# Kernel tuning notes

Hardware: AMD Instinct MI355X
Metric: run time of the kernel (lower is better)

## Reference

```python
import jax, jax.numpy as jnp
import numpy as np

B, N, E = 2, 2048, 1024   # batch, seq_len, embed_dim (= hidden_dim)
H, HD = 16, 64            # num_heads, head_dim


def setup_inputs() -> dict:
    key = jax.random.key(0)
    ks = jax.random.split(key, 6)
    w = lambda k: jax.random.normal(k, (E, E), jnp.float32) * 0.02
    return {
        "x": jax.random.normal(ks[0], (B, N, E), jnp.float32),
        "Wq": w(ks[1]), "bq": jnp.zeros((E,), jnp.float32),
        "Wk": w(ks[2]), "bk": jnp.zeros((E,), jnp.float32),
        "Wv": w(ks[3]), "bv": jnp.zeros((E,), jnp.float32),
        "Wu": w(ks[4]), "bu": jnp.zeros((E,), jnp.float32),
        "Wo": w(ks[5]), "bo": jnp.zeros((E,), jnp.float32),
        "ln_g": jnp.ones((E,), jnp.float32),
        "ln_b": jnp.zeros((E,), jnp.float32),
    }


def reference(x, Wq, bq, Wk, bk, Wv, bv, Wu, bu, Wo, bo, ln_g, ln_b):
    # projections (torch Linear: x @ W.T + b)
    q = x @ Wq.T + bq
    k = x @ Wk.T + bk
    v = jax.nn.silu(x @ Wv.T + bv)   # uv_act = swish
    u = jax.nn.silu(x @ Wu.T + bu)
    # split heads: [B, N, H*HD] -> [B, H, N, HD]
    split = lambda t: t.reshape(B, N, H, HD).transpose(0, 2, 1, 3)
    q, k, v = split(q), split(k), split(v)
    # non-softmax attention: ReLU on scaled energy (no causal mask)
    energy = jnp.einsum("bhnd,bhmd->bhnm", q, k) / jnp.float32(np.sqrt(HD))
    energy = jax.nn.relu(energy)
    out = jnp.einsum("bhnm,bhmd->bhnd", energy, v)
    # merge heads: [B, H, N, HD] -> [B, N, H*HD]
    out = out.transpose(0, 2, 1, 3).reshape(B, N, H * HD)
    # layernorm over hidden_dim
    mu = out.mean(-1, keepdims=True)
    var = out.var(-1, keepdims=True)
    out = (out - mu) * jax.lax.rsqrt(var + 1e-5) * ln_g + ln_b
    # gate and output projection
    out = u * out
    return out @ Wo.T + bo
```

## Files before the change

### kernel.cpp

```cpp
#include <hip/hip_runtime.h>
#include <stdint.h>

typedef unsigned short u16;
typedef __attribute__((ext_vector_type(8))) short short8;
typedef __attribute__((ext_vector_type(4))) short short4v;
typedef __attribute__((ext_vector_type(4))) float floatx4;
typedef __attribute__((ext_vector_type(4))) int intx4;

#define B_ 2
#define N_ 2048
#define E_ 1024
#define H_ 16
#define HD_ 64
#define M_TOT (B_ * N_)

__device__ __forceinline__ float bf2f(u16 h) {
    union { unsigned u; float f; } c; c.u = ((unsigned)h) << 16; return c.f;
}
__device__ __forceinline__ u16 f2bf(float f) {
    union { float f; unsigned u; } c; c.f = f;
    unsigned r = c.u + 0x7FFFu + ((c.u >> 16) & 1u);
    return (u16)(r >> 16);
}
__device__ __forceinline__ float silu_f(float x) { return x / (1.f + __expf(-x)); }

template <typename T> __device__ __forceinline__ void store_out(T* p, float v);
template <> __device__ __forceinline__ void store_out<u16>(u16* p, float v)    { *p = f2bf(v); }
template <> __device__ __forceinline__ void store_out<float>(float* p, float v) { *p = v; }

__device__ __forceinline__ void gll16(const void* g, void* l) {
    __builtin_amdgcn_global_load_lds(
        (const __attribute__((address_space(1))) void*)g,
        (__attribute__((address_space(3))) void*)l,
        16, 0, 0);
}

__device__ __forceinline__ short4v relu_pack(floatx4 s) {
    union { float f; unsigned u; } c0, c1, c2, c3;
    c0.f = fmaxf(s[0], 0.f); c1.f = fmaxf(s[1], 0.f);
    c2.f = fmaxf(s[2], 0.f); c3.f = fmaxf(s[3], 0.f);
    unsigned lo = __builtin_amdgcn_perm(c1.u + 0x8000u, c0.u + 0x8000u, 0x07060302);
    unsigned hi = __builtin_amdgcn_perm(c3.u + 0x8000u, c2.u + 0x8000u, 0x07060302);
    union { unsigned v[2]; short4v s4; } r; r.v[0] = lo; r.v[1] = hi;
    return r.s4;
}

__launch_bounds__(256, 4)
__global__ void cvt6(const float* __restrict__ s0, const float* __restrict__ s1,
                     const float* __restrict__ s2, const float* __restrict__ s3,
                     const float* __restrict__ s4, const float* __restrict__ s5,
                     u16* __restrict__ d0, u16* __restrict__ d1,
                     u16* __restrict__ d2, u16* __restrict__ d3,
                     u16* __restrict__ d4, u16* __restrict__ d5)
{
    const int z = blockIdx.z;
    if (z > 0 && blockIdx.x >= E_ * E_ / 2048) return;
    const float* src = (z == 0) ? s0 : (z == 1) ? s1 : (z == 2) ? s2
                     : (z == 3) ? s3 : (z == 4) ? s4 : s5;
    u16* dst         = (z == 0) ? d0 : (z == 1) ? d1 : (z == 2) ? d2
                     : (z == 3) ? d3 : (z == 4) ? d4 : d5;
    const int i = (blockIdx.x * 256 + threadIdx.x) * 8;
    floatx4 a = *(const floatx4*)(src + i);
    floatx4 b = *(const floatx4*)(src + i + 4);
    union { u16 h[8]; intx4 v; } o;
    o.h[0] = f2bf(a[0]); o.h[1] = f2bf(a[1]); o.h[2] = f2bf(a[2]); o.h[3] = f2bf(a[3]);
    o.h[4] = f2bf(b[0]); o.h[5] = f2bf(b[1]); o.h[6] = f2bf(b[2]); o.h[7] = f2bf(b[3]);
    *(intx4*)(dst + i) = o.v;
}

template <typename OutT>
__launch_bounds__(256, 2)
__global__ void gemm4(const u16* __restrict__ A,
                      const u16* __restrict__ W0, const u16* __restrict__ W1,
                      const u16* __restrict__ W2, const u16* __restrict__ W3,
                      const float* __restrict__ bi0, const float* __restrict__ bi1,
                      const float* __restrict__ bi2, const float* __restrict__ bi3,
                      OutT* __restrict__ O0, OutT* __restrict__ O1,
                      OutT* __restrict__ O2, OutT* __restrict__ O3,
                      int actmask, int scalemask, int K)
{
    __shared__ u16 a_lds[128 * 32];
    __shared__ u16 b_lds[128 * 32];

    const int lin = blockIdx.x + blockIdx.y * 8 + blockIdx.z * 256;
    const int swz = (lin & 7) * 128 + (lin >> 3);
    const int z   = swz >> 8;
    const int by  = (swz >> 3) & 31;
    const int bx  = swz & 7;

    const u16* W    = (z == 0) ? W0 : (z == 1) ? W1 : (z == 2) ? W2 : W3;
    const float* Bi = (z == 0) ? bi0 : (z == 1) ? bi1 : (z == 2) ? bi2 : bi3;
    OutT* Out       = (z == 0) ? O0 : (z == 1) ? O1 : (z == 2) ? O2 : O3;
    const bool act = (actmask >> z) & 1;
    const float osc = ((scalemask >> z) & 1) ? 0.125f : 1.0f;

    const int t    = threadIdx.x;
    const int wave = t >> 6, lane = t & 63, quad = lane >> 4, l16 = lane & 15;
    const int wm = wave >> 1, wn = wave & 1;
    const int m0 = by * 128;
    const int n0 = bx * 128;

    floatx4 acc[4][4];
    const floatx4 fz = {0.f, 0.f, 0.f, 0.f};
    for (int i = 0; i < 4; i++)
        for (int j = 0; j < 4; j++) acc[i][j] = fz;

    const int ar = t >> 2;
    const int ac = (t & 3) * 8;
    const u16* Ag0 = A + (size_t)(m0 + ar) * K + ac;
    const u16* Ag1 = A + (size_t)(m0 + 64 + ar) * K + ac;
    const u16* Bg0 = W + (size_t)(n0 + ar) * K + ac;
    const u16* Bg1 = W + (size_t)(n0 + 64 + ar) * K + ac;
    u16* al0 = a_lds + wave * 512;
    u16* al1 = a_lds + 2048 + wave * 512;
    u16* bl0 = b_lds + wave * 512;
    u16* bl1 = b_lds + 2048 + wave * 512;

    for (int k0 = 0; k0 < K; k0 += 32) {
        __syncthreads();
        gll16(Ag0 + k0, al0);
        gll16(Ag1 + k0, al1);
        gll16(Bg0 + k0, bl0);
        gll16(Bg1 + k0, bl1);
        __syncthreads();

        short8 af[4], bfr[4];
        for (int i = 0; i < 4; i++)
            af[i]  = *(const short8*)&a_lds[(wm * 64 + i * 16 + l16) * 32 + quad * 8];
        for (int j = 0; j < 4; j++)
            bfr[j] = *(const short8*)&b_lds[(wn * 64 + j * 16 + l16) * 32 + quad * 8];
        for (int i = 0; i < 4; i++)
            for (int j = 0; j < 4; j++)
                acc[i][j] = __builtin_amdgcn_mfma_f32_16x16x32_bf16(af[i], bfr[j], acc[i][j], 0, 0, 0);
    }

    float bias_v[4];
    for (int j = 0; j < 4; j++) bias_v[j] = Bi[n0 + wn * 64 + j * 16 + l16];

    for (int i = 0; i < 4; i++) {
        const int row = m0 + wm * 64 + i * 16 + quad * 4;
        for (int j = 0; j < 4; j++) {
            const int col = n0 + wn * 64 + j * 16 + l16;
            for (int r = 0; r < 4; r++) {
                float v = acc[i][j][r] + bias_v[j];
                if (act) v = silu_f(v);
                v *= osc;
                store_out<OutT>(&Out[(size_t)(row + r) * E_ + col], v);
            }
        }
    }
}

__launch_bounds__(256, 2)
__global__ void gemm_out(const u16* __restrict__ A, const u16* __restrict__ W,
                         const float* __restrict__ Bi, float* __restrict__ Out,
                         int K)
{
    __shared__ u16 a_lds[3][64 * 32];
    __shared__ u16 b_lds[3][128 * 32];

    const int t    = threadIdx.x;
    const int wave = t >> 6, lane = t & 63, quad = lane >> 4, l16 = lane & 15;
    const int m0 = blockIdx.y * 64;
    const int n0 = blockIdx.x * 128;

    floatx4 acc[4][2];
    const floatx4 fz = {0.f, 0.f, 0.f, 0.f};
    for (int i = 0; i < 4; i++)
        for (int j = 0; j < 2; j++) acc[i][j] = fz;

    const int ar = t >> 2;
    const int ac = (t & 3) * 8;
    const u16* Ag0 = A + (size_t)(m0 + ar) * K + ac;
    const u16* Bg0 = W + (size_t)(n0 + ar) * K + ac;
    const u16* Bg1 = W + (size_t)(n0 + 64 + ar) * K + ac;

    const int nt = K / 32;

#define GO_STAGE(tt, bi) {                                      \
        gll16(Ag0 + (tt) * 32, &a_lds[bi][wave * 512]);         \
        gll16(Bg0 + (tt) * 32, &b_lds[bi][wave * 512]);         \
        gll16(Bg1 + (tt) * 32, &b_lds[bi][2048 + wave * 512]); }

    GO_STAGE(0, 0);
    GO_STAGE(1, 1);
    asm volatile("s_waitcnt vmcnt(3)" ::: "memory");
    __builtin_amdgcn_s_barrier();

    for (int tt = 0; tt < nt; tt++) {
        const int bi = tt % 3;
        if (tt + 2 < nt) {
            GO_STAGE(tt + 2, (tt + 2) % 3);
        }
        short8 af[4], bfr[2];
#pragma unroll
        for (int i = 0; i < 4; i++)
            af[i]  = *(const short8*)&a_lds[bi][(i * 16 + l16) * 32 + quad * 8];
#pragma unroll
        for (int j = 0; j < 2; j++)
            bfr[j] = *(const short8*)&b_lds[bi][(wave * 32 + j * 16 + l16) * 32 + quad * 8];
#pragma unroll
        for (int i = 0; i < 4; i++)
#pragma unroll
            for (int j = 0; j < 2; j++)
                acc[i][j] = __builtin_amdgcn_mfma_f32_16x16x32_bf16(af[i], bfr[j], acc[i][j], 0, 0, 0);
        if (tt + 2 < nt) {
            asm volatile("s_waitcnt vmcnt(3)" ::: "memory");
        } else {
            asm volatile("s_waitcnt vmcnt(0)" ::: "memory");
        }
        __builtin_amdgcn_s_barrier();
    }
#undef GO_STAGE

    float bias_v[2];
    for (int j = 0; j < 2; j++) bias_v[j] = Bi[n0 + wave * 32 + j * 16 + l16];

    for (int i = 0; i < 4; i++) {
        const int row = m0 + i * 16 + quad * 4;
        for (int j = 0; j < 2; j++) {
            const int col = n0 + wave * 32 + j * 16 + l16;
            for (int r = 0; r < 4; r++)
                Out[(size_t)(row + r) * E_ + col] = acc[i][j][r] + bias_v[j];
        }
    }
}

#define LK 72
#define LV 72
#define KSPLIT 2
#define KCHUNK (N_ / KSPLIT)
#define NKT (KCHUNK / 64)

__launch_bounds__(256, 2)
__global__ void attn(const u16* __restrict__ Q, const u16* __restrict__ Kk,
                     const u16* __restrict__ V,
                     u16* __restrict__ P0, u16* __restrict__ P1)
{
    __shared__ u16 k_lds[2][64 * LK];
    __shared__ u16 v_lds[2][64 * LV];

    const int lin = blockIdx.x + blockIdx.y * 8 + blockIdx.z * 256;
    const int swz = (lin & 7) * 64 + (lin >> 3);
    const int z   = swz >> 8;
    const int bh  = (swz >> 3) & 31;
    const int qb  = swz & 7;

    const int b = bh >> 4, h = bh & 15;
    u16* __restrict__ Oa = (z == 0) ? P0 : P1;
    const int key_base = z * KCHUNK;

    const int t = threadIdx.x;
    const int wave = t >> 6, lane = t & 63, quad = lane >> 4, l16 = lane & 15;
    const int q0 = qb * 256 + wave * 64;
    const size_t base = (size_t)b * N_ * E_ + h * HD_;

    short8 aq[4][2];
    for (int mi = 0; mi < 4; mi++)
        for (int ks = 0; ks < 2; ks++)
            aq[mi][ks] = *(const short8*)(Q + base + (size_t)(q0 + mi * 16 + l16) * E_ + ks * 32 + quad * 8);

    floatx4 o[4][4];
    const floatx4 fz = {0.f, 0.f, 0.f, 0.f};
    for (int mi = 0; mi < 4; mi++)
        for (int nd = 0; nd < 4; nd++) o[mi][nd] = fz;

    const int srow = t >> 2, sseg = (t & 3) * 16;
    const int prow = (srow & 32) + (((srow >> 2) & 1) << 4)
                   + (((srow >> 3) & 3) << 2) + (srow & 3);
    const u16* Ksrc = Kk + base + (size_t)(key_base + srow) * E_ + sseg;
    const u16* Vsrc = V + base + (size_t)(key_base + srow) * E_ + sseg;
    const int kofs = prow * LK + sseg;

    intx4 kv0 = *(const intx4*)(Ksrc);
    intx4 kv1 = *(const intx4*)(Ksrc + 8);
    intx4 vv0 = *(const intx4*)(Vsrc);
    intx4 vv1 = *(const intx4*)(Vsrc + 8);
    {
        *(intx4*)(&k_lds[0][kofs])     = kv0;
        *(intx4*)(&k_lds[0][kofs + 8]) = kv1;
        const u16* v0p = (const u16*)&vv0;
        const u16* v1p = (const u16*)&vv1;
        for (int i = 0; i < 8; i++) {
            v_lds[0][(sseg + i) * LV + srow]     = v0p[i];
            v_lds[0][(sseg + 8 + i) * LV + srow] = v1p[i];
        }
    }

    for (int kt = 0; kt < NKT; kt++) {
        __syncthreads();
        const int cur = kt & 1;

        if (kt + 1 < NKT) {
            const u16* kg = Ksrc + (size_t)((kt + 1) * 64) * E_;
            const u16* vg = Vsrc + (size_t)((kt + 1) * 64) * E_;
            kv0 = *(const intx4*)(kg);
            kv1 = *(const intx4*)(kg + 8);
            vv0 = *(const intx4*)(vg);
            vv1 = *(const intx4*)(vg + 8);
        }

        for (int g = 0; g < 2; g++) {
            short8 ka[2][2];
            for (int tp = 0; tp < 2; tp++)
                for (int ks = 0; ks < 2; ks++)
                    ka[tp][ks] = *(const short8*)&k_lds[cur][(g * 32 + tp * 16 + l16) * LK + ks * 32 + quad * 8];
            short8 bv[4];
            for (int nd = 0; nd < 4; nd++)
                bv[nd] = *(const short8*)&v_lds[cur][(nd * 16 + l16) * LV + g * 32 + quad * 8];

            for (int mi = 0; mi < 4; mi++) {
                floatx4 c0 = __builtin_amdgcn_mfma_f32_16x16x32_bf16(ka[0][0], aq[mi][0], fz, 0, 0, 0);
                c0 = __builtin_amdgcn_mfma_f32_16x16x32_bf16(ka[0][1], aq[mi][1], c0, 0, 0, 0);
                floatx4 c1 = __builtin_amdgcn_mfma_f32_16x16x32_bf16(ka[1][0], aq[mi][0], fz, 0, 0, 0);
                c1 = __builtin_amdgcn_mfma_f32_16x16x32_bf16(ka[1][1], aq[mi][1], c1, 0, 0, 0);
                union { short4v h[2]; short8 s8; } sf;
                sf.h[0] = relu_pack(c0);
                sf.h[1] = relu_pack(c1);
                for (int nd = 0; nd < 4; nd++)
                    o[mi][nd] = __builtin_amdgcn_mfma_f32_16x16x32_bf16(sf.s8, bv[nd], o[mi][nd], 0, 0, 0);
            }
        }

        if (kt + 1 < NKT) {
            const int nxt = cur ^ 1;
            *(intx4*)(&k_lds[nxt][kofs])     = kv0;
            *(intx4*)(&k_lds[nxt][kofs + 8]) = kv1;
            const u16* v0p = (const u16*)&vv0;
            const u16* v1p = (const u16*)&vv1;
            for (int i = 0; i < 8; i++) {
                v_lds[nxt][(sseg + i) * LV + srow]     = v0p[i];
                v_lds[nxt][(sseg + 8 + i) * LV + srow] = v1p[i];
            }
        }
    }

    for (int mi = 0; mi < 4; mi++)
        for (int nd = 0; nd < 4; nd++)
            for (int r = 0; r < 4; r++)
                Oa[(size_t)(b * N_ + q0 + mi * 16 + quad * 4 + r) * E_ + h * HD_ + nd * 16 + l16] =
                    f2bf(o[mi][nd][r]);
}

__launch_bounds__(256, 4)
__global__ void ln_gate(const u16* __restrict__ P0, const u16* __restrict__ P1,
                        const u16* __restrict__ U,
                        const float* __restrict__ G, const float* __restrict__ Bb,
                        u16* __restrict__ Out)
{
    const int row = blockIdx.x;
    const int t = threadIdx.x;
    const size_t idx = (size_t)row * E_ + t * 4;
    const short4v a0 = *(const short4v*)(P0 + idx);
    const short4v a1 = *(const short4v*)(P1 + idx);
    floatx4 v;
    for (int i = 0; i < 4; i++)
        v[i] = bf2f((u16)a0[i]) + bf2f((u16)a1[i]);
    float s  = v[0] + v[1] + v[2] + v[3];
    float ss = v[0] * v[0] + v[1] * v[1] + v[2] * v[2] + v[3] * v[3];
    for (int off = 32; off; off >>= 1) {
        s  += __shfl_down(s, off, 64);
        ss += __shfl_down(ss, off, 64);
    }
    __shared__ float red[8];
    const int wave = t >> 6, lane = t & 63;
    if (lane == 0) { red[wave] = s; red[4 + wave] = ss; }
    __syncthreads();
    const float S  = red[0] + red[1] + red[2] + red[3];
    const float SS = red[4] + red[5] + red[6] + red[7];
    const float mu  = S * (1.f / E_);
    const float var = SS * (1.f / E_) - mu * mu;
    const float rstd = rsqrtf(var + 1e-5f);

    short4v outv;
    for (int i = 0; i < 4; i++) {
        const int e = t * 4 + i;
        float y = (v[i] - mu) * rstd * G[e] + Bb[e];
        y *= bf2f(U[idx + i]);
        outv[i] = (short)f2bf(y);
    }
    *(short4v*)(Out + idx) = outv;
}

extern "C" void kernel_launch(void* const* d_in, const int* in_sizes, int n_in,
                              void* d_out, int out_size, void* d_ws, size_t ws_size,
                              hipStream_t stream)
{
    const float* x   = (const float*)d_in[0];
    const float* Wq  = (const float*)d_in[1];
    const float* bq  = (const float*)d_in[2];
    const float* Wk  = (const float*)d_in[3];
    const float* bk  = (const float*)d_in[4];
    const float* Wv  = (const float*)d_in[5];
    const float* bv  = (const float*)d_in[6];
    const float* Wu  = (const float*)d_in[7];
    const float* bu  = (const float*)d_in[8];
    const float* Wo  = (const float*)d_in[9];
    const float* bo  = (const float*)d_in[10];
    const float* lng = (const float*)d_in[11];
    const float* lnb = (const float*)d_in[12];

    char* ws = (char*)d_ws;
    u16*  qw  = (u16*)(ws);
    u16*  kw  = (u16*)(ws + 8388608);
    u16*  vw  = (u16*)(ws + 16777216);
    u16*  uw  = (u16*)(ws + 25165824);
    u16*  p0  = (u16*)(ws + 33554432);
    u16*  p1  = (u16*)(ws + 41943040);
    u16*  xb  = (u16*)(ws + 50331648);
    u16*  wbq = (u16*)(ws + 58720256);
    u16*  wbk = (u16*)(ws + 60817408);
    u16*  wbv = (u16*)(ws + 62914560);
    u16*  wbu = (u16*)(ws + 65011712);
    u16*  wbo = (u16*)(ws + 67108864);
    u16*  gw  = (u16*)(ws);

    float* out = (float*)d_out;

    cvt6<<<dim3(M_TOT * E_ / 2048, 1, 6), dim3(256, 1, 1), 0, stream>>>(
        x, Wq, Wk, Wv, Wu, Wo, xb, wbq, wbk, wbv, wbu, wbo);
    gemm4<u16><<<dim3(8, 32, 4), dim3(256, 1, 1), 0, stream>>>(
        xb, wbq, wbk, wbv, wbu, bq, bk, bv, bu, qw, kw, vw, uw, 0xC, 0x1, E_);
    attn<<<dim3(N_ / 256, B_ * H_, KSPLIT), dim3(256, 1, 1), 0, stream>>>(qw, kw, vw, p0, p1);
    ln_gate<<<dim3(M_TOT, 1, 1), dim3(256, 1, 1), 0, stream>>>(p0, p1, uw, lng, lnb, gw);
    gemm_out<<<dim3(E_ / 128, M_TOT / 64, 1), dim3(256, 1, 1), 0, stream>>>(gw, wbo, bo, out, E_);
}
```

Measured before the change: 213.4 us.

## Split QKVU projection into large-tile Q/K GEMM and raise attention key split

```diff
diff --git a/kernel.cpp b/kernel.cpp
--- a/kernel.cpp
+++ b/kernel.cpp
@@ -68,6 +68,127 @@
     *(intx4*)(dst + i) = o.v;
 }
 
+#define NT8 (E_ / 64)
+
+__launch_bounds__(512, 2)
+__global__ void gemm8p2(const u16* __restrict__ A,
+                        const u16* __restrict__ W0, const u16* __restrict__ W1,
+                        const float* __restrict__ bi0, const float* __restrict__ bi1,
+                        u16* __restrict__ O0, u16* __restrict__ O1,
+                        int scalemask)
+{
+    __shared__ u16 lds[65536];
+
+    const int z = blockIdx.z;
+    const u16* Wp   = z ? W1 : W0;
+    const float* Bi = z ? bi1 : bi0;
+    u16* Out        = z ? O1 : O0;
+    const float osc = ((scalemask >> z) & 1) ? 0.125f : 1.0f;
+
+    const int tid = threadIdx.x;
+    const int wid = tid >> 6, lane = tid & 63, quad = lane >> 4, l16 = lane & 15;
+    const int wm = wid >> 2, wn = wid & 3;
+    const int m0 = blockIdx.y * 256;
+    const int n0 = blockIdx.x * 256;
+
+    const int swz = ((l16 >> 3) & 1) * 16;
+    const int raA = wm * 8192 + l16 * 32 + ((quad * 8) ^ swz);
+    const int raB = (wn >> 1) * 8192 + ((wn & 1) * 64 + l16) * 32 + ((quad * 8) ^ swz);
+
+    const int srow_s = tid >> 2;
+    const int sce = ((tid & 3) * 8) ^ (((tid >> 5) & 1) * 16);
+    const u16* As = A  + (size_t)(m0 + srow_s) * E_ + sce;
+    const u16* Bs = Wp + (size_t)(n0 + srow_s) * E_ + sce;
+
+#define ST_A8(t, h, bufx) if ((t) < NT8) {                                                      \
+        gll16(As + (size_t)(h)*128*E_ + (t)*64,      &lds[(bufx)*16384 + (h)*8192 + wid*512]);  \
+        gll16(As + (size_t)(h)*128*E_ + (t)*64 + 32, &lds[(bufx)*16384 + (h)*8192 + 4096 + wid*512]); }
+#define ST_B8(t, h, bufx) if ((t) < NT8) {                                                      \
+        gll16(Bs + (size_t)(h)*128*E_ + (t)*64,      &lds[32768 + (bufx)*16384 + (h)*8192 + wid*512]);  \
+        gll16(Bs + (size_t)(h)*128*E_ + (t)*64 + 32, &lds[32768 + (bufx)*16384 + (h)*8192 + 4096 + wid*512]); }
+
+    floatx4 acc[8][4];
+    const floatx4 fz = {0.f, 0.f, 0.f, 0.f};
+#pragma unroll
+    for (int mi = 0; mi < 8; mi++)
+#pragma unroll
+        for (int bn = 0; bn < 4; bn++) acc[mi][bn] = fz;
+
+    short8 af[8][2], bfr[2][2];
+
+#define RD_A8(mlo, bufx)                                                               \
+    _Pragma("unroll")                                                                  \
+    for (int mi = 0; mi < 4; mi++) {                                                   \
+        af[(mlo)+mi][0] = *(const short8*)&lds[(bufx)*16384 + raA + ((mlo)+mi)*512];   \
+        af[(mlo)+mi][1] = *(const short8*)&lds[(bufx)*16384 + raA + 4096 + ((mlo)+mi)*512]; }
+#define RD_B8(blo, bufx)                                                               \
+    _Pragma("unroll")                                                                  \
+    for (int bn = 0; bn < 2; bn++) {                                                   \
+        bfr[bn][0] = *(const short8*)&lds[32768 + (bufx)*16384 + raB + ((blo)+bn)*512];   \
+        bfr[bn][1] = *(const short8*)&lds[32768 + (bufx)*16384 + raB + 4096 + ((blo)+bn)*512]; }
+#define MF8(mlo, blo)                                                                  \
+    _Pragma("unroll")                                                                  \
+    for (int mi = 0; mi < 4; mi++)                                                     \
+        _Pragma("unroll")                                                              \
+        for (int bn = 0; bn < 2; bn++) {                                               \
+            acc[(mlo)+mi][(blo)+bn] = __builtin_amdgcn_mfma_f32_16x16x32_bf16(         \
+                af[(mlo)+mi][0], bfr[bn][0], acc[(mlo)+mi][(blo)+bn], 0, 0, 0);        \
+            acc[(mlo)+mi][(blo)+bn] = __builtin_amdgcn_mfma_f32_16x16x32_bf16(         \
+                af[(mlo)+mi][1], bfr[bn][1], acc[(mlo)+mi][(blo)+bn], 0, 0, 0); }
+
+    ST_A8(0, 0, 0); ST_A8(0, 1, 0); ST_B8(0, 0, 0); ST_B8(0, 1, 0);
+    ST_A8(1, 0, 1);
+    asm volatile("s_waitcnt vmcnt(2)" ::: "memory");
+    __builtin_amdgcn_s_barrier();
+
+    for (int t = 0; t < NT8; t++) {
+        const int buf = t & 1, ob = buf ^ 1;
+        RD_A8(0, buf); RD_B8(0, buf);
+        ST_A8(t + 1, 1, ob);
+        __builtin_amdgcn_s_setprio(1); MF8(0, 0); __builtin_amdgcn_s_setprio(0);
+        __builtin_amdgcn_s_barrier();
+        RD_A8(4, buf);
+        ST_B8(t + 1, 0, ob);
+        __builtin_amdgcn_s_setprio(1); MF8(4, 0); __builtin_amdgcn_s_setprio(0);
+        __builtin_amdgcn_s_barrier();
+        RD_B8(2, buf);
+        ST_B8(t + 1, 1, ob);
+        __builtin_amdgcn_s_setprio(1); MF8(4, 2); __builtin_amdgcn_s_setprio(0);
+        __builtin_amdgcn_s_barrier();
+        ST_A8(t + 2, 0, buf);
+        __builtin_amdgcn_s_setprio(1); MF8(0, 2); __builtin_amdgcn_s_setprio(0);
+        if (t + 2 < NT8) {
+            asm volatile("s_waitcnt vmcnt(2)" ::: "memory");
+        } else {
+            asm volatile("s_waitcnt vmcnt(0)" ::: "memory");
+        }
+        __builtin_amdgcn_s_barrier();
+    }
+#undef ST_A8
+#undef ST_B8
+#undef RD_A8
+#undef RD_B8
+#undef MF8
+
+    float bias_v[4];
+#pragma unroll
+    for (int bn = 0; bn < 4; bn++) bias_v[bn] = Bi[n0 + wn * 64 + bn * 16 + l16];
+
+#pragma unroll
+    for (int mi = 0; mi < 8; mi++) {
+        const int row = m0 + wm * 128 + mi * 16 + quad * 4;
+#pragma unroll
+        for (int bn = 0; bn < 4; bn++) {
+            const int col = n0 + wn * 64 + bn * 16 + l16;
+#pragma unroll
+            for (int r = 0; r < 4; r++) {
+                float v = (acc[mi][bn][r] + bias_v[bn]) * osc;
+                Out[(size_t)(row + r) * E_ + col] = f2bf(v);
+            }
+        }
+    }
+}
+
 template <typename OutT>
 __launch_bounds__(256, 2)
 __global__ void gemm4(const u16* __restrict__ A,
@@ -82,12 +203,7 @@
     __shared__ u16 a_lds[128 * 32];
     __shared__ u16 b_lds[128 * 32];
 
-    const int lin = blockIdx.x + blockIdx.y * 8 + blockIdx.z * 256;
-    const int swz = (lin & 7) * 128 + (lin >> 3);
-    const int z   = swz >> 8;
-    const int by  = (swz >> 3) & 31;
-    const int bx  = swz & 7;
-
+    const int z = blockIdx.z;
     const u16* W    = (z == 0) ? W0 : (z == 1) ? W1 : (z == 2) ? W2 : W3;
     const float* Bi = (z == 0) ? bi0 : (z == 1) ? bi1 : (z == 2) ? bi2 : bi3;
     OutT* Out       = (z == 0) ? O0 : (z == 1) ? O1 : (z == 2) ? O2 : O3;
@@ -97,8 +213,8 @@
     const int t    = threadIdx.x;
     const int wave = t >> 6, lane = t & 63, quad = lane >> 4, l16 = lane & 15;
     const int wm = wave >> 1, wn = wave & 1;
-    const int m0 = by * 128;
-    const int n0 = bx * 128;
+    const int m0 = blockIdx.y * 128;
+    const int n0 = blockIdx.x * 128;
 
     floatx4 acc[4][4];
     const floatx4 fz = {0.f, 0.f, 0.f, 0.f};
@@ -228,26 +344,27 @@
 
 #define LK 72
 #define LV 72
-#define KSPLIT 2
+#define KSPLIT 4
 #define KCHUNK (N_ / KSPLIT)
 #define NKT (KCHUNK / 64)
 
-__launch_bounds__(256, 2)
+__launch_bounds__(256, 4)
 __global__ void attn(const u16* __restrict__ Q, const u16* __restrict__ Kk,
                      const u16* __restrict__ V,
-                     u16* __restrict__ P0, u16* __restrict__ P1)
+                     u16* __restrict__ P0, u16* __restrict__ P1,
+                     u16* __restrict__ P2, u16* __restrict__ P3)
 {
     __shared__ u16 k_lds[2][64 * LK];
     __shared__ u16 v_lds[2][64 * LV];
 
     const int lin = blockIdx.x + blockIdx.y * 8 + blockIdx.z * 256;
-    const int swz = (lin & 7) * 64 + (lin >> 3);
+    const int swz = (lin & 7) * 128 + (lin >> 3);
     const int z   = swz >> 8;
     const int bh  = (swz >> 3) & 31;
     const int qb  = swz & 7;
 
     const int b = bh >> 4, h = bh & 15;
-    u16* __restrict__ Oa = (z == 0) ? P0 : P1;
+    u16* __restrict__ Oa = (z == 0) ? P0 : (z == 1) ? P1 : (z == 2) ? P2 : P3;
     const int key_base = z * KCHUNK;
 
     const int t = threadIdx.x;
@@ -344,6 +461,7 @@
 
 __launch_bounds__(256, 4)
 __global__ void ln_gate(const u16* __restrict__ P0, const u16* __restrict__ P1,
+                        const u16* __restrict__ P2, const u16* __restrict__ P3,
                         const u16* __restrict__ U,
                         const float* __restrict__ G, const float* __restrict__ Bb,
                         u16* __restrict__ Out)
@@ -353,9 +471,11 @@
     const size_t idx = (size_t)row * E_ + t * 4;
     const short4v a0 = *(const short4v*)(P0 + idx);
     const short4v a1 = *(const short4v*)(P1 + idx);
+    const short4v a2 = *(const short4v*)(P2 + idx);
+    const short4v a3 = *(const short4v*)(P3 + idx);
     floatx4 v;
     for (int i = 0; i < 4; i++)
-        v[i] = bf2f((u16)a0[i]) + bf2f((u16)a1[i]);
+        v[i] = bf2f((u16)a0[i]) + bf2f((u16)a1[i]) + bf2f((u16)a2[i]) + bf2f((u16)a3[i]);
     float s  = v[0] + v[1] + v[2] + v[3];
     float ss = v[0] * v[0] + v[1] * v[1] + v[2] * v[2] + v[3] * v[3];
     for (int off = 32; off; off >>= 1) {
@@ -416,12 +536,18 @@
     u16*  gw  = (u16*)(ws);
 
     float* out = (float*)d_out;
+    u16*  p2  = (u16*)d_out;
+    u16*  p3  = (u16*)d_out + 4194304;
 
     cvt6<<<dim3(M_TOT * E_ / 2048, 1, 6), dim3(256, 1, 1), 0, stream>>>(
         x, Wq, Wk, Wv, Wu, Wo, xb, wbq, wbk, wbv, wbu, wbo);
-    gemm4<u16><<<dim3(8, 32, 4), dim3(256, 1, 1), 0, stream>>>(
-        xb, wbq, wbk, wbv, wbu, bq, bk, bv, bu, qw, kw, vw, uw, 0xC, 0x1, E_);
-    attn<<<dim3(N_ / 256, B_ * H_, KSPLIT), dim3(256, 1, 1), 0, stream>>>(qw, kw, vw, p0, p1);
-    ln_gate<<<dim3(M_TOT, 1, 1), dim3(256, 1, 1), 0, stream>>>(p0, p1, uw, lng, lnb, gw);
+    gemm8p2<<<dim3(E_ / 256, M_TOT / 256, 2), dim3(512, 1, 1), 0, stream>>>(
+        xb, wbq, wbk, bq, bk, qw, kw, 0x1);
+    gemm4<u16><<<dim3(8, 32, 2), dim3(256, 1, 1), 0, stream>>>(
+        xb, wbv, wbu, wbv, wbu, bv, bu, bv, bu, vw, uw, vw, uw, 0x3, 0x0, E_);
+    attn<<<dim3(N_ / 256, B_ * H_, KSPLIT), dim3(256, 1, 1), 0, stream>>>(
+        qw, kw, vw, p0, p1, p2, p3);
+    ln_gate<<<dim3(M_TOT, 1, 1), dim3(256, 1, 1), 0, stream>>>(
+        p0, p1, p2, p3, uw, lng, lnb, gw);
     gemm_out<<<dim3(E_ / 128, M_TOT / 64, 1), dim3(256, 1, 1), 0, stream>>>(gw, wbo, bo, out, E_);
 }
```

Result: slower. 339.3 us (+59.0%).
